# Kernel optimization log

Measured on AMD Instinct MI355X. Metric: run time of the kernel, lower is better.

The kernel has to match this reference:

```python
import jax, jax.numpy as jnp
import numpy as np

N_NODES = 100000

def gcn_conv(x, edge_index, W, b):
    # torch_geometric GCNConv: add self-loops, sym-normalize, aggregate, add bias
    n = x.shape[0]
    loop = jnp.arange(n)
    src = jnp.concatenate([edge_index[0], loop])  # [E+N]
    dst = jnp.concatenate([edge_index[1], loop])
    h = x @ W  # [N, out]
    deg = jax.ops.segment_sum(jnp.ones_like(dst, dtype=h.dtype), dst, num_segments=n)
    dinv = jnp.where(deg > 0, jax.lax.rsqrt(deg), 0.0)
    norm = dinv[src] * dinv[dst]  # [E+N]
    msg = h[src] * norm[:, None]  # gather + scale
    out = jax.ops.segment_sum(msg, dst, num_segments=n)  # scatter-add
    return out + b

def setup_inputs() -> dict:
    key = jax.random.key(0)
    ks = jax.random.split(key, 6)
    N, F, H, C, E = N_NODES, 128, 128, 32, 1600000
    x = jax.random.normal(ks[0], (N, F), dtype=jnp.float32)
    edge_index = jax.random.randint(ks[1], (2, E), 0, N, dtype=jnp.int64)
    W1 = jax.random.normal(ks[2], (F, H), dtype=jnp.float32) * (1.0 / np.sqrt(F))
    b1 = jnp.zeros((H,), jnp.float32)
    W2 = jax.random.normal(ks[3], (H, H), dtype=jnp.float32) * (1.0 / np.sqrt(H))
    b2 = jnp.zeros((H,), jnp.float32)
    Wc = jax.random.normal(ks[4], (H, C), dtype=jnp.float32) * (1.0 / np.sqrt(H))
    bc = jnp.zeros((C,), jnp.float32)
    return {"x": x, "edge_index": edge_index, "W1": W1, "b1": b1, "W2": W2, "b2": b2, "Wc": Wc, "bc": bc}

def reference(x, edge_index, W1, b1, W2, b2, Wc, bc):
    h = jax.nn.relu(gcn_conv(x, edge_index, W1, b1))
    # dropout is identity in eval mode
    h = jax.nn.relu(gcn_conv(h, edge_index, W2, b2))
    pooled = jnp.mean(h, axis=0)  # [H]
    return pooled @ Wc + bc  # [C]
```

## Files before the change

kernel.cpp:

```cpp
#include <hip/hip_runtime.h>
#include <hip/hip_bf16.h>


#define FEAT 128
#define CHUNK 4096
#define MAXBUCK 512
#define ECAP 12288
#define PBLK 512

typedef __attribute__((ext_vector_type(8))) short short8;
typedef __attribute__((ext_vector_type(4))) float float4v;
typedef __attribute__((ext_vector_type(2))) float floatx2;

union I4S8 { int4 i; short8 s; };

static __device__ inline unsigned short f2bf(float f) {
    union { __hip_bfloat16 h; unsigned short u; } cv;
    cv.h = __float2bfloat16(f);
    return cv.u;
}

static __device__ inline floatx2 fp8x2_dec(unsigned int u) {
#if __has_builtin(__builtin_amdgcn_cvt_pk_f32_fp8)
    return __builtin_amdgcn_cvt_pk_f32_fp8((int)u, false);
#else
    floatx2 r;
    unsigned int b0 = u & 0xFFu, b1 = (u >> 8) & 0xFFu;
    r.x = __uint_as_float(((b0 & 0x80u) << 24) | ((b0 & 0x7Fu) << 20)) * 0x1p+120f;
    r.y = __uint_as_float(((b1 & 0x80u) << 24) | ((b1 & 0x7Fu) << 20)) * 0x1p+120f;
    return r;
#endif
}

static __device__ inline floatx2 fp8x2_dec_hi(unsigned int u) {
#if __has_builtin(__builtin_amdgcn_cvt_pk_f32_fp8)
    return __builtin_amdgcn_cvt_pk_f32_fp8((int)u, true);
#else
    return fp8x2_dec(u >> 16);
#endif
}

static __device__ inline unsigned short fp8x2_enc(float x, float y) {
#if __has_builtin(__builtin_amdgcn_cvt_pk_fp8_f32)
    return (unsigned short)(__builtin_amdgcn_cvt_pk_fp8_f32(x, y, 0, false) & 0xFFFF);
#else
    auto enc1 = [](float f) -> unsigned int {
        unsigned int u = __float_as_uint(f);
        unsigned int s = (u >> 24) & 0x80u;
        float a = fabsf(f);
        a = fminf(a, 448.0f);
        unsigned int code;
        if (a < 0.015625f) {
            code = (unsigned int)(int)rintf(a * 512.0f);
        } else {
            unsigned int au = __float_as_uint(a);
            unsigned int r = au + 0x0007FFFFu + ((au >> 20) & 1u);
            unsigned int e = (r >> 23) - 120u;
            unsigned int m = (r >> 20) & 7u;
            code = (e << 3) | m;
            if (code > 0x7Eu) code = 0x7Eu;
        }
        return code | s;
    };
    return (unsigned short)(enc1(x) | (enc1(y) << 8));
#endif
}

static __device__ inline unsigned char fp8enc(float f) {
#if __has_builtin(__builtin_amdgcn_cvt_pk_fp8_f32)
    return (unsigned char)(__builtin_amdgcn_cvt_pk_fp8_f32(f, 0.0f, 0, false) & 0xFF);
#else
    return (unsigned char)(fp8x2_enc(f, 0.0f) & 0xFF);
#endif
}

__global__ __launch_bounds__(256) void hist2(const int* __restrict__ dst,
                                             int* __restrict__ hist,
                                             int nE, int NC, int nbuck) {
    __shared__ int h[MAXBUCK];
    int c = blockIdx.x, t = threadIdx.x;
    for (int i = t; i < nbuck; i += 256) h[i] = 0;
    __syncthreads();
    int beg = c * CHUNK, end = min(nE, beg + CHUNK);
    for (int e = beg + t; e < end; e += 256)
        atomicAdd(&h[dst[e] >> 8], 1);
    __syncthreads();
    for (int i = t; i < nbuck; i += 256) hist[i * NC + c] = h[i];
}

__global__ __launch_bounds__(256) void rowsum_k(const int* __restrict__ hist,
                                                int* __restrict__ btot, int NC) {
    __shared__ int red[256];
    int b = blockIdx.x, t = threadIdx.x;
    int s = 0;
    for (int c = t; c < NC; c += 256) s += hist[b * NC + c];
    red[t] = s;
    __syncthreads();
    for (int o = 128; o > 0; o >>= 1) {
        if (t < o) red[t] += red[t + o];
        __syncthreads();
    }
    if (t == 0) btot[b] = red[0];
}

__global__ __launch_bounds__(512) void bscan_k(const int* __restrict__ btot,
                                               int* __restrict__ bboff, int nbuck) {
    __shared__ int sc[512];
    int t = threadIdx.x;
    int v = (t < nbuck) ? btot[t] : 0;
    sc[t] = v;
    __syncthreads();
    for (int o = 1; o < 512; o <<= 1) {
        int add = (t >= o) ? sc[t - o] : 0;
        __syncthreads();
        sc[t] += add;
        __syncthreads();
    }
    if (t < nbuck) {
        bboff[t] = sc[t] - v;
        if (t == nbuck - 1) bboff[nbuck] = sc[t];
    }
}

__global__ __launch_bounds__(512) void rowoff_k(const int* __restrict__ hist,
                                                const int* __restrict__ bboff,
                                                int* __restrict__ hoff, int NC) {
    __shared__ int sc[512];
    int b = blockIdx.x, t = threadIdx.x;
    int v = (t < NC) ? hist[b * NC + t] : 0;
    sc[t] = v;
    __syncthreads();
    for (int o = 1; o < 512; o <<= 1) {
        int add = (t >= o) ? sc[t - o] : 0;
        __syncthreads();
        sc[t] += add;
        __syncthreads();
    }
    if (t < NC) hoff[b * NC + t] = bboff[b] + sc[t] - v;
}

__global__ __launch_bounds__(256) void fill2(const int* __restrict__ src,
                                             const int* __restrict__ dst,
                                             const int* __restrict__ off,
                                             int* __restrict__ binned,
                                             int nE, int NC, int nbuck) {
    __shared__ int cur[MAXBUCK];
    int c = blockIdx.x, t = threadIdx.x;
    for (int i = t; i < nbuck; i += 256) cur[i] = off[i * NC + c];
    __syncthreads();
    int beg = c * CHUNK, end = min(nE, beg + CHUNK);
    for (int e = beg + t; e < end; e += 256) {
        int d = dst[e];
        int pos = atomicAdd(&cur[d >> 8], 1);
        binned[pos] = (src[e] << 8) | (d & 255);
    }
}

__global__ __launch_bounds__(256) void bucket_scat(const int* __restrict__ binned,
                                                   const int* __restrict__ bboff,
                                                   int* __restrict__ cnt,
                                                   float* __restrict__ dinv,
                                                   int* __restrict__ cursor,
                                                   int* __restrict__ csr_src, int n) {
    __shared__ int se[ECAP];
    __shared__ int lcnt[256];
    __shared__ int lcur[256];
    __shared__ int ssc[256];
    int b = blockIdx.x, t = threadIdx.x;
    int node0 = b << 8;
    int nloc = min(256, n - node0);
    int ebeg = bboff[b], eend = bboff[b + 1];
    int ne = eend - ebeg;
    lcnt[t] = 0;
    __syncthreads();
    bool staged = (ne <= ECAP);
    if (staged) {
        for (int i = t; i < ne; i += 256) {
            int e = binned[ebeg + i];
            se[i] = e;
            atomicAdd(&lcnt[e & 255], 1);
        }
    } else {
        for (int i = t; i < ne; i += 256)
            atomicAdd(&lcnt[binned[ebeg + i] & 255], 1);
    }
    __syncthreads();
    int myc = (t < nloc) ? lcnt[t] : 0;
    ssc[t] = myc;
    __syncthreads();
    for (int o = 1; o < 256; o <<= 1) {
        int add = (t >= o) ? ssc[t - o] : 0;
        __syncthreads();
        ssc[t] += add;
        __syncthreads();
    }
    int excl = ssc[t] - myc;
    if (t < nloc) {
        cnt[node0 + t] = myc;
        dinv[node0 + t] = rsqrtf((float)(myc + 1));
        cursor[node0 + t] = ebeg + excl;
        lcur[t] = excl;
    }
    __syncthreads();
    if (staged) {
        for (int i = t; i < ne; i += 256) {
            int e = se[i];
            int pos = atomicAdd(&lcur[e & 255], 1);
            csr_src[ebeg + pos] = ((unsigned int)e) >> 8;
        }
    } else {
        for (int i = t; i < ne; i += 256) {
            int e = binned[ebeg + i];
            int pos = atomicAdd(&lcur[e & 255], 1);
            csr_src[ebeg + pos] = ((unsigned int)e) >> 8;
        }
    }
}

__global__ __launch_bounds__(256) void wprep2(const float* __restrict__ W1,
                                              const float* __restrict__ W2,
                                              unsigned short* __restrict__ Wbf1,
                                              unsigned short* __restrict__ Wbf2) {
    int tid = blockIdx.x * 256 + threadIdx.x;
    const float* W = (tid < 16384) ? W1 : W2;
    unsigned short* O = (tid < 16384) ? Wbf1 : Wbf2;
    int id = tid & 16383;
    int chunk = id >> 3, j = id & 7;
    int kb = chunk >> 7, nn = chunk & 127;
    O[id] = f2bf(W[(kb * 8 + j) * FEAT + nn]);
}

template <bool AFP32>
__global__ __launch_bounds__(256) void gemm_mfma(const void* __restrict__ Xv,
                                                 const unsigned short* __restrict__ Wbf,
                                                 const float* __restrict__ dinv,
                                                 unsigned char* __restrict__ gout,
                                                 int n) {
    int wave = threadIdx.x >> 6, lane = threadIdx.x & 63;
    int m0 = blockIdx.x * 64 + wave * 16;
    if (m0 >= n) return;
    int col = lane & 15, quad = lane >> 4;
    int mc = min(m0 + col, n - 1);

    short8 afr[4];
    if (AFP32) {
        const float* X = (const float*)Xv;
        const float* xr = X + (size_t)mc * FEAT + quad * 8;
#pragma unroll
        for (int ks = 0; ks < 4; ks++) {
            float4 lo = *(const float4*)(xr + ks * 32);
            float4 hi = *(const float4*)(xr + ks * 32 + 4);
            short8 a;
            a[0] = (short)f2bf(lo.x); a[1] = (short)f2bf(lo.y);
            a[2] = (short)f2bf(lo.z); a[3] = (short)f2bf(lo.w);
            a[4] = (short)f2bf(hi.x); a[5] = (short)f2bf(hi.y);
            a[6] = (short)f2bf(hi.z); a[7] = (short)f2bf(hi.w);
            afr[ks] = a;
        }
    } else {
        const unsigned char* X8 = (const unsigned char*)Xv;
        const unsigned char* xr = X8 + (size_t)mc * FEAT + quad * 8;
#pragma unroll
        for (int ks = 0; ks < 4; ks++) {
            uint2 u2 = *(const uint2*)(xr + ks * 32);
            floatx2 p0 = fp8x2_dec(u2.x);
            floatx2 p1 = fp8x2_dec_hi(u2.x);
            floatx2 p2 = fp8x2_dec(u2.y);
            floatx2 p3 = fp8x2_dec_hi(u2.y);
            short8 a;
            a[0] = (short)f2bf(p0.x); a[1] = (short)f2bf(p0.y);
            a[2] = (short)f2bf(p1.x); a[3] = (short)f2bf(p1.y);
            a[4] = (short)f2bf(p2.x); a[5] = (short)f2bf(p2.y);
            a[6] = (short)f2bf(p3.x); a[7] = (short)f2bf(p3.y);
            afr[ks] = a;
        }
    }

    float dvr[4];
#pragma unroll
    for (int r = 0; r < 4; r++)
        dvr[r] = dinv[min(m0 + quad * 4 + r, n - 1)];

    const int4* Wb = (const int4*)Wbf;
#pragma unroll
    for (int nt = 0; nt < 8; nt++) {
        float4v acc = {0.f, 0.f, 0.f, 0.f};
#pragma unroll
        for (int ks = 0; ks < 4; ks++) {
            int kb = ks * 4 + quad;
            I4S8 u; u.i = Wb[kb * FEAT + nt * 16 + col];
            acc = __builtin_amdgcn_mfma_f32_16x16x32_bf16(afr[ks], u.s, acc, 0, 0, 0);
        }
#pragma unroll
        for (int r = 0; r < 4; r++) {
            int row = m0 + quad * 4 + r;
            if (row < n)
                gout[(size_t)row * FEAT + nt * 16 + col] = fp8enc(acc[r] * dvr[r]);
        }
    }
}

static __device__ inline void gather_node(const unsigned char* __restrict__ csrB,
                                          const unsigned char* __restrict__ gb,
                                          int beg, int end, unsigned node,
                                          unsigned lane2, float& sx, float& sy) {
    floatx2 a0 = fp8x2_dec(*(const unsigned short*)(gb + ((node << 7) | lane2)));
    floatx2 a1 = {0.f, 0.f}, a2 = {0.f, 0.f}, a3 = {0.f, 0.f};
    int j = beg;
    for (; j + 15 < end; j += 16) {
        unsigned jb = (unsigned)j << 2;
        unsigned sIdx[16];
#pragma unroll
        for (int k = 0; k < 16; k++)
            sIdx[k] = *(const unsigned*)(csrB + (jb + 4u * (unsigned)k));
        unsigned short uu[16];
#pragma unroll
        for (int k = 0; k < 16; k++)
            uu[k] = *(const unsigned short*)(gb + ((sIdx[k] << 7) | lane2));
#pragma unroll
        for (int k = 0; k < 16; k += 4) {
            a0 += fp8x2_dec(uu[k]);
            a1 += fp8x2_dec(uu[k + 1]);
            a2 += fp8x2_dec(uu[k + 2]);
            a3 += fp8x2_dec(uu[k + 3]);
        }
    }
    for (; j + 3 < end; j += 4) {
        unsigned jb = (unsigned)j << 2;
        unsigned s0 = *(const unsigned*)(csrB + jb);
        unsigned s1 = *(const unsigned*)(csrB + (jb + 4u));
        unsigned s2 = *(const unsigned*)(csrB + (jb + 8u));
        unsigned s3 = *(const unsigned*)(csrB + (jb + 12u));
        a0 += fp8x2_dec(*(const unsigned short*)(gb + ((s0 << 7) | lane2)));
        a1 += fp8x2_dec(*(const unsigned short*)(gb + ((s1 << 7) | lane2)));
        a2 += fp8x2_dec(*(const unsigned short*)(gb + ((s2 << 7) | lane2)));
        a3 += fp8x2_dec(*(const unsigned short*)(gb + ((s3 << 7) | lane2)));
    }
    for (; j < end; j++) {
        unsigned s0 = *(const unsigned*)(csrB + ((unsigned)j << 2));
        a0 += fp8x2_dec(*(const unsigned short*)(gb + ((s0 << 7) | lane2)));
    }
    floatx2 a = (a0 + a1) + (a2 + a3);
    sx = a.x;
    sy = a.y;
}

__global__ __launch_bounds__(256) void agg_csr(const int* __restrict__ cursor,
                                               const int* __restrict__ cnt,
                                               const int* __restrict__ csr_src,
                                               const unsigned char* __restrict__ gbuf,
                                               const float* __restrict__ dinv,
                                               const float* __restrict__ bias,
                                               unsigned short* __restrict__ outb,
                                               int n) {
    int node = blockIdx.x * 4 + (threadIdx.x >> 6);
    if (node >= n) return;
    unsigned lane = threadIdx.x & 63;
    unsigned lane2 = lane << 1;
    int beg = cursor[node];
    int end = beg + cnt[node];
    float sx, sy;
    gather_node((const unsigned char*)csr_src, gbuf, beg, end,
                (unsigned)node, lane2, sx, sy);
    float dv = dinv[node];
    float2 bv = ((const float2*)bias)[lane];
    float rx = fmaxf(sx * dv + bv.x, 0.0f);
    float ry = fmaxf(sy * dv + bv.y, 0.0f);
    outb[(((unsigned)node) << 6) | lane] = fp8x2_enc(rx, ry);
}

__global__ __launch_bounds__(256) void pool_kernel(const unsigned char* __restrict__ a,
                                                   float* __restrict__ partial, int n) {
    __shared__ float red[16][132];
    int t = threadIdx.x, b = blockIdx.x;
    int fg = t & 15;
    int rg = t >> 4;
    unsigned fb = (unsigned)fg << 3;
    floatx2 s01 = {0.f, 0.f}, s23 = {0.f, 0.f}, s45 = {0.f, 0.f}, s67 = {0.f, 0.f};
    for (int i = (b << 4) | rg; i < n; i += PBLK * 16) {
        uint2 u2 = *(const uint2*)(a + (((unsigned)i << 7) | fb));
        s01 += fp8x2_dec(u2.x);
        s23 += fp8x2_dec_hi(u2.x);
        s45 += fp8x2_dec(u2.y);
        s67 += fp8x2_dec_hi(u2.y);
    }
    red[rg][fb + 0] = s01.x; red[rg][fb + 1] = s01.y;
    red[rg][fb + 2] = s23.x; red[rg][fb + 3] = s23.y;
    red[rg][fb + 4] = s45.x; red[rg][fb + 5] = s45.y;
    red[rg][fb + 6] = s67.x; red[rg][fb + 7] = s67.y;
    __syncthreads();
    if (t < FEAT) {
        float s = 0.0f;
#pragma unroll
        for (int k = 0; k < 16; k++) s += red[k][t];
        partial[b * FEAT + t] = s;
    }
}

__global__ __launch_bounds__(128) void final_kernel(const float* __restrict__ partial,
                                                    const float* __restrict__ Wc,
                                                    const float* __restrict__ bc,
                                                    float* __restrict__ out,
                                                    int n, int C) {
    __shared__ float p[FEAT];
    int t = threadIdx.x;
    float s = 0.0f;
    for (int b = 0; b < PBLK; b++) s += partial[b * FEAT + t];
    p[t] = s * (1.0f / (float)n);
    __syncthreads();
    if (t < C) {
        float acc = bc[t];
        for (int h = 0; h < FEAT; h++)
            acc += p[h] * Wc[h * C + t];
        out[t] = acc;
    }
}

extern "C" void kernel_launch(void* const* d_in, const int* in_sizes, int n_in,
                              void* d_out, int out_size, void* d_ws, size_t ws_size,
                              hipStream_t stream) {
    const float* x  = (const float*)d_in[0];
    const int*   ei = (const int*)d_in[1];
    const float* W1 = (const float*)d_in[2];
    const float* b1 = (const float*)d_in[3];
    const float* W2 = (const float*)d_in[4];
    const float* b2 = (const float*)d_in[5];
    const float* Wc = (const float*)d_in[6];
    const float* bc = (const float*)d_in[7];

    const int N = in_sizes[0] / FEAT;
    const int E = in_sizes[1] / 2;
    const int C = out_size;
    const int* srcI = ei;
    const int* dstI = ei + E;
    const int NC = (E + CHUNK - 1) / CHUNK;
    const int NBK = (N + 255) >> 8;

    auto align256 = [](size_t v) { return (v + 255) & ~(size_t)255; };
    char* w = (char*)d_ws;
    int*            cnt     = (int*)w;            w += align256((size_t)N * 4);
    float*          dinv    = (float*)w;          w += align256((size_t)N * 4);
    int*            cursor  = (int*)w;            w += align256((size_t)N * 4);
    int*            csr_src = (int*)w;            w += align256((size_t)E * 4);
    int*            binned  = (int*)w;            w += align256((size_t)E * 4);
    int*            hist    = (int*)w;            w += align256((size_t)NBK * NC * 4);
    int*            hoff    = (int*)w;            w += align256((size_t)NBK * NC * 4);
    int*            btot    = (int*)w;            w += align256((size_t)NBK * 4);
    int*            bboff   = (int*)w;            w += align256((size_t)(NBK + 1) * 4);
    unsigned short* Wbf1    = (unsigned short*)w; w += align256((size_t)FEAT * FEAT * 2);
    unsigned short* Wbf2    = (unsigned short*)w; w += align256((size_t)FEAT * FEAT * 2);
    unsigned char*  gbuf    = (unsigned char*)w;  w += align256((size_t)N * FEAT);
    unsigned char*  bufA    = (unsigned char*)w;  w += align256((size_t)N * FEAT);
    float*          partial = (float*)w;          w += align256((size_t)PBLK * FEAT * 4);

    wprep2<<<128, 256, 0, stream>>>(W1, W2, Wbf1, Wbf2);

    hist2<<<NC, 256, 0, stream>>>(dstI, hist, E, NC, NBK);
    rowsum_k<<<NBK, 256, 0, stream>>>(hist, btot, NC);
    bscan_k<<<1, 512, 0, stream>>>(btot, bboff, NBK);
    rowoff_k<<<NBK, 512, 0, stream>>>(hist, bboff, hoff, NC);
    fill2<<<NC, 256, 0, stream>>>(srcI, dstI, hoff, binned, E, NC, NBK);
    bucket_scat<<<NBK, 256, 0, stream>>>(binned, bboff, cnt, dinv, cursor, csr_src, N);

    const int gGemm = (N + 63) / 64;
    const int gAgg = (N + 3) / 4;

    gemm_mfma<true><<<gGemm, 256, 0, stream>>>(x, Wbf1, dinv, gbuf, N);
    agg_csr<<<gAgg, 256, 0, stream>>>(cursor, cnt, csr_src, gbuf, dinv, b1,
                                      (unsigned short*)bufA, N);

    gemm_mfma<false><<<gGemm, 256, 0, stream>>>(bufA, Wbf2, dinv, gbuf, N);
    agg_csr<<<gAgg, 256, 0, stream>>>(cursor, cnt, csr_src, gbuf, dinv, b2,
                                      (unsigned short*)bufA, N);

    pool_kernel<<<PBLK, 256, 0, stream>>>(bufA, partial, N);
    final_kernel<<<1, 128, 0, stream>>>(partial, Wc, bc, (float*)d_out, N, C);
}
```

Baseline: 312.3 us.

## Pad CSR rows to multiples of 16 with zero-row sentinel and vector index loads

Each node's CSR neighbor list is padded to a multiple of 16 entries, and the padding points at an extra all-zero row appended to the feature buffer. Source indices are stored pre-shifted to byte offsets. The aggregation kernel can then run a single unrolled loop of 16 with four int4 index loads and wave-uniform bounds, with no remainder loops. In exchange, padding adds extra gathers from the zero row (on average about 7.5 per node) and adds CSR storage and per-thread padding writes in the build kernel.

```diff
diff --git a/kernel.cpp b/kernel.cpp
--- a/kernel.cpp
+++ b/kernel.cpp
@@ -7,6 +7,7 @@
 #define MAXBUCK 512
 #define ECAP 12288
 #define PBLK 512
+#define BPAD 3856
 
 typedef __attribute__((ext_vector_type(8))) short short8;
 typedef __attribute__((ext_vector_type(4))) float float4v;
@@ -171,6 +172,8 @@
     int nloc = min(256, n - node0);
     int ebeg = bboff[b], eend = bboff[b + 1];
     int ne = eend - ebeg;
+    int pbase = (ebeg + b * BPAD + 15) & ~15;
+    int zOff = n << 7;
     lcnt[t] = 0;
     __syncthreads();
     bool staged = (ne <= ECAP);
@@ -186,7 +189,8 @@
     }
     __syncthreads();
     int myc = (t < nloc) ? lcnt[t] : 0;
-    ssc[t] = myc;
+    int mycp = (myc + 15) & ~15;
+    ssc[t] = mycp;
     __syncthreads();
     for (int o = 1; o < 256; o <<= 1) {
         int add = (t >= o) ? ssc[t - o] : 0;
@@ -194,34 +198,42 @@
         ssc[t] += add;
         __syncthreads();
     }
-    int excl = ssc[t] - myc;
+    int exclp = ssc[t] - mycp;
     if (t < nloc) {
-        cnt[node0 + t] = myc;
+        cnt[node0 + t] = mycp;
         dinv[node0 + t] = rsqrtf((float)(myc + 1));
-        cursor[node0 + t] = ebeg + excl;
-        lcur[t] = excl;
+        cursor[node0 + t] = pbase + exclp;
+        lcur[t] = exclp;
     }
     __syncthreads();
     if (staged) {
         for (int i = t; i < ne; i += 256) {
             int e = se[i];
             int pos = atomicAdd(&lcur[e & 255], 1);
-            csr_src[ebeg + pos] = ((unsigned int)e) >> 8;
+            csr_src[pbase + pos] = (int)(((unsigned int)e >> 8) << 7);
         }
     } else {
         for (int i = t; i < ne; i += 256) {
             int e = binned[ebeg + i];
             int pos = atomicAdd(&lcur[e & 255], 1);
-            csr_src[ebeg + pos] = ((unsigned int)e) >> 8;
-        }
+            csr_src[pbase + pos] = (int)(((unsigned int)e >> 8) << 7);
+        }
+    }
+    if (t < nloc) {
+        for (int i = exclp + myc; i < exclp + mycp; i++)
+            csr_src[pbase + i] = zOff;
     }
 }
 
 __global__ __launch_bounds__(256) void wprep2(const float* __restrict__ W1,
                                               const float* __restrict__ W2,
                                               unsigned short* __restrict__ Wbf1,
-                                              unsigned short* __restrict__ Wbf2) {
+                                              unsigned short* __restrict__ Wbf2,
+                                              unsigned char* __restrict__ gbuf,
+                                              int n) {
     int tid = blockIdx.x * 256 + threadIdx.x;
+    if (tid < 32)
+        ((unsigned int*)(gbuf + (size_t)n * FEAT))[tid] = 0u;
     const float* W = (tid < 16384) ? W1 : W2;
     unsigned short* O = (tid < 16384) ? Wbf1 : Wbf2;
     int id = tid & 16383;
@@ -300,51 +312,6 @@
     }
 }
 
-static __device__ inline void gather_node(const unsigned char* __restrict__ csrB,
-                                          const unsigned char* __restrict__ gb,
-                                          int beg, int end, unsigned node,
-                                          unsigned lane2, float& sx, float& sy) {
-    floatx2 a0 = fp8x2_dec(*(const unsigned short*)(gb + ((node << 7) | lane2)));
-    floatx2 a1 = {0.f, 0.f}, a2 = {0.f, 0.f}, a3 = {0.f, 0.f};
-    int j = beg;
-    for (; j + 15 < end; j += 16) {
-        unsigned jb = (unsigned)j << 2;
-        unsigned sIdx[16];
-#pragma unroll
-        for (int k = 0; k < 16; k++)
-            sIdx[k] = *(const unsigned*)(csrB + (jb + 4u * (unsigned)k));
-        unsigned short uu[16];
-#pragma unroll
-        for (int k = 0; k < 16; k++)
-            uu[k] = *(const unsigned short*)(gb + ((sIdx[k] << 7) | lane2));
-#pragma unroll
-        for (int k = 0; k < 16; k += 4) {
-            a0 += fp8x2_dec(uu[k]);
-            a1 += fp8x2_dec(uu[k + 1]);
-            a2 += fp8x2_dec(uu[k + 2]);
-            a3 += fp8x2_dec(uu[k + 3]);
-        }
-    }
-    for (; j + 3 < end; j += 4) {
-        unsigned jb = (unsigned)j << 2;
-        unsigned s0 = *(const unsigned*)(csrB + jb);
-        unsigned s1 = *(const unsigned*)(csrB + (jb + 4u));
-        unsigned s2 = *(const unsigned*)(csrB + (jb + 8u));
-        unsigned s3 = *(const unsigned*)(csrB + (jb + 12u));
-        a0 += fp8x2_dec(*(const unsigned short*)(gb + ((s0 << 7) | lane2)));
-        a1 += fp8x2_dec(*(const unsigned short*)(gb + ((s1 << 7) | lane2)));
-        a2 += fp8x2_dec(*(const unsigned short*)(gb + ((s2 << 7) | lane2)));
-        a3 += fp8x2_dec(*(const unsigned short*)(gb + ((s3 << 7) | lane2)));
-    }
-    for (; j < end; j++) {
-        unsigned s0 = *(const unsigned*)(csrB + ((unsigned)j << 2));
-        a0 += fp8x2_dec(*(const unsigned short*)(gb + ((s0 << 7) | lane2)));
-    }
-    floatx2 a = (a0 + a1) + (a2 + a3);
-    sx = a.x;
-    sy = a.y;
-}
-
 __global__ __launch_bounds__(256) void agg_csr(const int* __restrict__ cursor,
                                                const int* __restrict__ cnt,
                                                const int* __restrict__ csr_src,
@@ -357,15 +324,49 @@
     if (node >= n) return;
     unsigned lane = threadIdx.x & 63;
     unsigned lane2 = lane << 1;
-    int beg = cursor[node];
-    int end = beg + cnt[node];
-    float sx, sy;
-    gather_node((const unsigned char*)csr_src, gbuf, beg, end,
-                (unsigned)node, lane2, sx, sy);
+    int begS = __builtin_amdgcn_readfirstlane(cursor[node]);
+    int endS = begS + __builtin_amdgcn_readfirstlane(cnt[node]);
+    const unsigned char* csrB = (const unsigned char*)csr_src;
+
+    floatx2 a0 = fp8x2_dec(*(const unsigned short*)(gbuf + ((((unsigned)node) << 7) | lane2)));
+    floatx2 a1 = {0.f, 0.f}, a2 = {0.f, 0.f}, a3 = {0.f, 0.f};
+
+    for (int j = begS; j < endS; j += 16) {
+        const unsigned char* p = csrB + ((size_t)(unsigned)j << 2);
+        int4 w0 = *(const int4*)(p);
+        int4 w1 = *(const int4*)(p + 16);
+        int4 w2 = *(const int4*)(p + 32);
+        int4 w3 = *(const int4*)(p + 48);
+        unsigned short uu[16];
+        uu[0]  = *(const unsigned short*)(gbuf + ((unsigned)w0.x | lane2));
+        uu[1]  = *(const unsigned short*)(gbuf + ((unsigned)w0.y | lane2));
+        uu[2]  = *(const unsigned short*)(gbuf + ((unsigned)w0.z | lane2));
+        uu[3]  = *(const unsigned short*)(gbuf + ((unsigned)w0.w | lane2));
+        uu[4]  = *(const unsigned short*)(gbuf + ((unsigned)w1.x | lane2));
+        uu[5]  = *(const unsigned short*)(gbuf + ((unsigned)w1.y | lane2));
+        uu[6]  = *(const unsigned short*)(gbuf + ((unsigned)w1.z | lane2));
+        uu[7]  = *(const unsigned short*)(gbuf + ((unsigned)w1.w | lane2));
+        uu[8]  = *(const unsigned short*)(gbuf + ((unsigned)w2.x | lane2));
+        uu[9]  = *(const unsigned short*)(gbuf + ((unsigned)w2.y | lane2));
+        uu[10] = *(const unsigned short*)(gbuf + ((unsigned)w2.z | lane2));
+        uu[11] = *(const unsigned short*)(gbuf + ((unsigned)w2.w | lane2));
+        uu[12] = *(const unsigned short*)(gbuf + ((unsigned)w3.x | lane2));
+        uu[13] = *(const unsigned short*)(gbuf + ((unsigned)w3.y | lane2));
+        uu[14] = *(const unsigned short*)(gbuf + ((unsigned)w3.z | lane2));
+        uu[15] = *(const unsigned short*)(gbuf + ((unsigned)w3.w | lane2));
+#pragma unroll
+        for (int k = 0; k < 16; k += 4) {
+            a0 += fp8x2_dec(uu[k]);
+            a1 += fp8x2_dec(uu[k + 1]);
+            a2 += fp8x2_dec(uu[k + 2]);
+            a3 += fp8x2_dec(uu[k + 3]);
+        }
+    }
+    floatx2 a = (a0 + a1) + (a2 + a3);
     float dv = dinv[node];
     float2 bv = ((const float2*)bias)[lane];
-    float rx = fmaxf(sx * dv + bv.x, 0.0f);
-    float ry = fmaxf(sy * dv + bv.y, 0.0f);
+    float rx = fmaxf(a.x * dv + bv.x, 0.0f);
+    float ry = fmaxf(a.y * dv + bv.y, 0.0f);
     outb[(((unsigned)node) << 6) | lane] = fp8x2_enc(rx, ry);
 }
 
@@ -435,13 +436,14 @@
     const int* dstI = ei + E;
     const int NC = (E + CHUNK - 1) / CHUNK;
     const int NBK = (N + 255) >> 8;
+    const size_t csrCap = (size_t)E + (size_t)NBK * BPAD + 64;
 
     auto align256 = [](size_t v) { return (v + 255) & ~(size_t)255; };
     char* w = (char*)d_ws;
     int*            cnt     = (int*)w;            w += align256((size_t)N * 4);
     float*          dinv    = (float*)w;          w += align256((size_t)N * 4);
     int*            cursor  = (int*)w;            w += align256((size_t)N * 4);
-    int*            csr_src = (int*)w;            w += align256((size_t)E * 4);
+    int*            csr_src = (int*)w;            w += align256(csrCap * 4);
     int*            binned  = (int*)w;            w += align256((size_t)E * 4);
     int*            hist    = (int*)w;            w += align256((size_t)NBK * NC * 4);
     int*            hoff    = (int*)w;            w += align256((size_t)NBK * NC * 4);
@@ -449,11 +451,11 @@
     int*            bboff   = (int*)w;            w += align256((size_t)(NBK + 1) * 4);
     unsigned short* Wbf1    = (unsigned short*)w; w += align256((size_t)FEAT * FEAT * 2);
     unsigned short* Wbf2    = (unsigned short*)w; w += align256((size_t)FEAT * FEAT * 2);
-    unsigned char*  gbuf    = (unsigned char*)w;  w += align256((size_t)N * FEAT);
+    unsigned char*  gbuf    = (unsigned char*)w;  w += align256((size_t)(N + 1) * FEAT);
     unsigned char*  bufA    = (unsigned char*)w;  w += align256((size_t)N * FEAT);
     float*          partial = (float*)w;          w += align256((size_t)PBLK * FEAT * 4);
 
-    wprep2<<<128, 256, 0, stream>>>(W1, W2, Wbf1, Wbf2);
+    wprep2<<<128, 256, 0, stream>>>(W1, W2, Wbf1, Wbf2, gbuf, N);
 
     hist2<<<NC, 256, 0, stream>>>(dstI, hist, E, NC, NBK);
     rowsum_k<<<NBK, 256, 0, stream>>>(hist, btot, NC);
```

After: 279.3 us. 10.6% less time.
